# Kernel optimization log

Hardware: AMD Instinct MI355X
Metric: run time of the kernel (lower is better)

## Reference

```python
import math
import jax, jax.numpy as jnp
import numpy as np

B, L, HID = 2, 2048, 2048
H = 16
D = HID // H  # 128
EPS = 1e-6
ROPE_BASE = 10000.0
BETA_MIN, BETA_MAX = 0.8, 0.9995


def _rope_cache(seq_len, dim):
    half = dim // 2
    inv_freq = 1.0 / (ROPE_BASE ** (jnp.arange(half, dtype=jnp.float32) / float(half)))
    t = jnp.arange(seq_len, dtype=jnp.float32)
    freqs = t[:, None] * inv_freq[None, :]  # [L, half]
    return jnp.cos(freqs), jnp.sin(freqs)


def _apply_rope(x, cos, sin):
    # x: [B, H, L, D]; cos/sin: [L, D//2]
    half = x.shape[-1] // 2
    xe, xo = x[..., :half], x[..., half:]
    c = cos[None, None]
    s = sin[None, None]
    return jnp.concatenate([xe * c - xo * s, xe * s + xo * c], axis=-1)


def setup_inputs() -> dict:
    key = jax.random.key(0)
    ks = jax.random.split(key, 6)
    sc = 1.0 / math.sqrt(HID)  # ~ xavier scale
    return {
        "x": jax.random.normal(ks[0], (B, L, HID), jnp.float32),
        "Wq": jax.random.normal(ks[1], (HID, HID), jnp.float32) * sc,
        "Wk": jax.random.normal(ks[2], (HID, HID), jnp.float32) * sc,
        "Wv": jax.random.normal(ks[3], (HID, HID), jnp.float32) * sc,
        "Wg": jax.random.normal(ks[4], (HID, H), jnp.float32) * sc,
        "bg": jnp.full((H,), math.log(0.98 / (1.0 - 0.98)), jnp.float32),
        "Wo": jax.random.normal(ks[5], (HID, HID), jnp.float32) * sc,
        "bo": jnp.zeros((HID,), jnp.float32),
    }


def _deltanet(x, Wq, Wk, Wv, Wg, bg, Wo, bo):
    Bb, Ll, _ = x.shape
    split = lambda t: t.reshape(Bb, Ll, H, D).transpose(0, 2, 1, 3)  # [B,H,L,D]
    q = split(x @ Wq)
    k = split(x @ Wk)
    v = split(x @ Wv)

    cos, sin = _rope_cache(Ll, D)
    q = _apply_rope(q, cos, sin)
    k = _apply_rope(k, cos, sin)

    beta = jax.nn.sigmoid(x @ Wg + bg)                # [B,L,H]
    beta = jnp.clip(beta, BETA_MIN, BETA_MAX).transpose(0, 2, 1)  # [B,H,L]

    phi_q = jax.nn.elu(q) + 1.0
    phi_k = jax.nn.elu(k) + 1.0

    # time-major for scan
    pq = phi_q.transpose(2, 0, 1, 3)  # [L,B,H,D]
    pk = phi_k.transpose(2, 0, 1, 3)
    vt = v.transpose(2, 0, 1, 3)
    bt = beta.transpose(2, 0, 1)      # [L,B,H]

    S0 = jnp.zeros((Bb, H, D, D), jnp.float32)
    z0 = jnp.zeros((Bb, H, D), jnp.float32)

    def step(carry, inp):
        S, z = carry
        pq_t, pk_t, v_t, b_t = inp
        S = S * b_t[..., None, None] + pk_t[..., :, None] * v_t[..., None, :]
        z = z * b_t[..., None] + pk_t
        numer = jnp.einsum('bhd,bhde->bhe', pq_t, S)
        denom = jnp.sum(pq_t * z, axis=-1, keepdims=True) + EPS
        return (S, z), numer / denom

    (_, _), y = jax.lax.scan(step, (S0, z0), (pq, pk, vt, bt))  # y: [L,B,H,D]
    y = y.transpose(1, 0, 2, 3).reshape(Bb, Ll, HID)  # [B,L,H*D]
    return y @ Wo + bo


def reference(x, Wq, Wk, Wv, Wg, bg, Wo, bo):
    return _deltanet(x, Wq, Wk, Wv, Wg, bg, Wo, bo)
```

## Files before the change

### kernel.cpp

```cpp
#include <hip/hip_runtime.h>


typedef __attribute__((ext_vector_type(8))) short short8;
typedef __attribute__((ext_vector_type(4))) float f32x4;

__device__ __forceinline__ unsigned short f2bf(float f) {
  unsigned u = __float_as_uint(f);
  u += 0x7fffu + ((u >> 16) & 1u);
  return (unsigned short)(u >> 16);
}
__device__ __forceinline__ float bf2f(unsigned short s) {
  return __uint_as_float(((unsigned)s) << 16);
}
__device__ __forceinline__ float phi_elu1(float x) {
  return x > 0.f ? x + 1.f : expf(x);
}
__device__ __forceinline__ void gl_lds16(const void* g, void* l) {
  __builtin_amdgcn_global_load_lds(
      (const __attribute__((address_space(1))) void*)g,
      (__attribute__((address_space(3))) void*)l, 16, 0, 0);
}
__device__ __forceinline__ void bar_raw() {
  asm volatile("" ::: "memory");
  __builtin_amdgcn_s_barrier();
  asm volatile("" ::: "memory");
}

__global__ __launch_bounds__(256)
void k_cast(const float* __restrict__ x, unsigned short* __restrict__ xb) {
  int i = (blockIdx.x * 256 + threadIdx.x) * 4;
  float4 f = *(const float4*)(x + i);
  uint2 p;
  p.x = (unsigned)f2bf(f.x) | ((unsigned)f2bf(f.y) << 16);
  p.y = (unsigned)f2bf(f.z) | ((unsigned)f2bf(f.w) << 16);
  *(uint2*)(xb + i) = p;
}

__global__ __launch_bounds__(256)
void k_transw(const float* __restrict__ Wq, const float* __restrict__ Wk,
              const float* __restrict__ Wv, const float* __restrict__ Wo,
              const float* __restrict__ Wg,
              unsigned short* __restrict__ Wt, unsigned short* __restrict__ Wot,
              unsigned short* __restrict__ Wgt16) {
  const int z = blockIdx.z;
  if (z == 4) {
    if (blockIdx.y != 0) return;
    int idx = blockIdx.x * 256 + threadIdx.x;
    int h = idx >> 9, k4 = (idx & 511) * 4;
    uint2 p;
    p.x = (unsigned)f2bf(Wg[(k4 + 0) * 16 + h]) | ((unsigned)f2bf(Wg[(k4 + 1) * 16 + h]) << 16);
    p.y = (unsigned)f2bf(Wg[(k4 + 2) * 16 + h]) | ((unsigned)f2bf(Wg[(k4 + 3) * 16 + h]) << 16);
    *(uint2*)(Wgt16 + (size_t)h * 2048 + k4) = p;
    return;
  }
  const float* W = (z == 0) ? Wq : (z == 1) ? Wk : (z == 2) ? Wv : Wo;
  unsigned short* out = (z < 3) ? (Wt + (size_t)z * 2048 * 2048) : Wot;
  __shared__ float tile[64][65];
  const int n0 = blockIdx.x * 64;
  const int k0 = blockIdx.y * 64;
  const int tx = threadIdx.x & 63;
  const int ty = threadIdx.x >> 6;
#pragma unroll
  for (int rl = 0; rl < 16; ++rl) {
    int kk = rl * 4 + ty;
    tile[kk][tx] = W[(size_t)(k0 + kk) * 2048 + n0 + tx];
  }
  __syncthreads();
#pragma unroll
  for (int rl = 0; rl < 16; ++rl) {
    int nn = rl * 4 + ty;
    out[(size_t)(n0 + nn) * 2048 + k0 + tx] = f2bf(tile[tx][nn]);
  }
}

__global__ __launch_bounds__(256)
void k_betaW(const unsigned short* __restrict__ xb, const unsigned short* __restrict__ Wgt16,
             const float* __restrict__ bg, float* __restrict__ beta) {
  const int w = threadIdx.x >> 6;
  const int lane = threadIdx.x & 63;
  const int m = blockIdx.x * 4 + w;
  const int h = lane & 15, kq = lane >> 4;
  const unsigned short* xr = xb + (size_t)m * 2048 + kq * 512;
  const unsigned short* wr = Wgt16 + (size_t)h * 2048 + kq * 512;
  float acc = 0.f;
#pragma unroll 8
  for (int i = 0; i < 64; ++i) {
    short8 xv = *(const short8*)(xr + i * 8);
    short8 wv = *(const short8*)(wr + i * 8);
#pragma unroll
    for (int j = 0; j < 8; ++j)
      acc = fmaf(bf2f((unsigned short)xv[j]), bf2f((unsigned short)wv[j]), acc);
  }
  acc += __shfl_xor(acc, 16, 64);
  acc += __shfl_xor(acc, 32, 64);
  if (lane < 16) {
    float v = acc + bg[h];
    float bv = 1.f / (1.f + expf(-v));
    beta[(size_t)m * 16 + h] = fminf(fmaxf(bv, 0.8f), 0.9995f);
  }
}

template <bool OUT_BF16, bool ADD_BIAS>
__global__ __launch_bounds__(512, 2)
void k_gemm2(const unsigned short* __restrict__ A, const unsigned short* __restrict__ Bt,
             void* __restrict__ Cptr, const float* __restrict__ bias,
             int M, int N, int K, int ldA, int ldC) {
  __shared__ __align__(16) unsigned short Ls[3][3][128][64];
  const int tid = threadIdx.x;
  const int lane = tid & 63;
  const int w = tid >> 6;
  const int wm = w >> 1;
  const int wn = w & 1;
  const int ql = lane >> 4;
  const int r = lane & 15;

  const int nwg = gridDim.x * gridDim.y;
  const int orig = blockIdx.y * gridDim.x + blockIdx.x;
  const int li = (orig & 7) * (nwg >> 3) + (orig >> 3);
  const int m0 = (li & 15) * 256;
  const int n0 = (li >> 4) * 128;

  const int srow = tid >> 3;
  const int sphys = tid & 7;
  const int slog = sphys ^ (srow & 7);
  const unsigned short* Ab = A + (size_t)(m0 + srow) * ldA + slog * 8;
  const unsigned short* Bb = Bt + (size_t)(n0 + srow) * K + slog * 8;

#define STG(st, h, tt)                                                        \
  do {                                                                        \
    const size_t ldx = ((h) == 2) ? (size_t)K : (size_t)ldA;                  \
    const unsigned short* gs =                                                \
        (((h) == 2) ? Bb : (Ab + (size_t)((h) * 128) * ldA)) +                \
        (size_t)(tt) * 64;                                                    \
    unsigned short* ld = &Ls[(st)][(h)][srow][sphys * 8];                     \
    gl_lds16(gs, ld);                                                         \
    gl_lds16(gs + 64 * ldx, ld + 64 * 64);                                    \
  } while (0)

  f32x4 acc[4][4];
#pragma unroll
  for (int i = 0; i < 4; ++i)
#pragma unroll
    for (int j = 0; j < 4; ++j) acc[i][j] = (f32x4){0.f, 0.f, 0.f, 0.f};

  const int NT = K >> 6;

#pragma unroll
  for (int h = 0; h < 3; ++h) STG(0, h, 0);
#pragma unroll
  for (int h = 0; h < 3; ++h) STG(1, h, 1);
  asm volatile("s_waitcnt vmcnt(6)" ::: "memory");
  bar_raw();

  short8 bfr[4][2];

  for (int t = 0; t < NT; ++t) {
    const int st = t % 3;
    const unsigned short (*LA)[64] = Ls[st][wm >> 1];
    const unsigned short (*LB)[64] = Ls[st][2];
    const int arow0 = (wm & 1) * 64;
    const int brow0 = wn * 64;
    const bool pf = (t + 2 < NT);
    const int s2 = (t + 2) % 3;
#pragma unroll
    for (int p = 0; p < 2; ++p) {
      if (p == 0) {
#pragma unroll
        for (int nj = 0; nj < 4; ++nj)
#pragma unroll
          for (int kk = 0; kk < 2; ++kk)
            bfr[nj][kk] = *(const short8*)
                &LB[brow0 + nj * 16 + r][((kk * 4 + ql) ^ (r & 7)) * 8];
      }
      short8 af[2][2];
#pragma unroll
      for (int im = 0; im < 2; ++im)
#pragma unroll
        for (int kk = 0; kk < 2; ++kk)
          af[im][kk] = *(const short8*)
              &LA[arow0 + (p * 2 + im) * 16 + r][((kk * 4 + ql) ^ (r & 7)) * 8];
      if (pf) {
        if (p == 0) {
          STG(s2, 0, t + 2);
          STG(s2, 1, t + 2);
        } else {
          STG(s2, 2, t + 2);
        }
      }
      bar_raw();
      asm volatile("s_waitcnt lgkmcnt(0)" ::: "memory");
      __builtin_amdgcn_sched_barrier(0);
      __builtin_amdgcn_s_setprio(1);
#pragma unroll
      for (int kk = 0; kk < 2; ++kk)
#pragma unroll
        for (int im = 0; im < 2; ++im)
#pragma unroll
          for (int nj = 0; nj < 4; ++nj)
            acc[p * 2 + im][nj] = __builtin_amdgcn_mfma_f32_16x16x32_bf16(
                af[im][kk], bfr[nj][kk], acc[p * 2 + im][nj], 0, 0, 0);
      __builtin_amdgcn_s_setprio(0);
      if (p == 1) {
        if (pf)
          asm volatile("s_waitcnt vmcnt(6)" ::: "memory");
        else if (t + 1 < NT)
          asm volatile("s_waitcnt vmcnt(0)" ::: "memory");
      }
      bar_raw();
    }
  }
#undef STG

#pragma unroll
  for (int mi = 0; mi < 4; ++mi) {
#pragma unroll
    for (int nj = 0; nj < 4; ++nj) {
#pragma unroll
      for (int rr = 0; rr < 4; ++rr) {
        int mrow = m0 + wm * 64 + mi * 16 + ql * 4 + rr;
        int ncol = n0 + wn * 64 + nj * 16 + r;
        float val = acc[mi][nj][rr];
        if (ADD_BIAS) val += bias[ncol];
        if (OUT_BF16)
          ((unsigned short*)Cptr)[(size_t)mrow * ldC + ncol] = f2bf(val);
        else
          ((float*)Cptr)[(size_t)mrow * ldC + ncol] = val;
      }
    }
  }
}

__global__ __launch_bounds__(256)
void k_prep(const unsigned short* __restrict__ qkv, const float* __restrict__ beta,
            unsigned short* __restrict__ Qt, unsigned short* __restrict__ Ktg,
            unsigned short* __restrict__ Ag, float* __restrict__ gch) {
  const int ch = blockIdx.x;
  const int bh = blockIdx.y;
  const int b = bh >> 4, h = bh & 15;
  const int tid = threadIdx.x;
  const int t0 = ch * 64;

  __shared__ float Gs[64];
  __shared__ unsigned short Qs[64][136];
  __shared__ unsigned short Ks[64][136];

  if (tid < 64) {
    float bb = beta[((size_t)(b * 2048 + t0 + tid)) * 16 + h];
#pragma unroll
    for (int off = 1; off < 64; off <<= 1) {
      float o = __shfl_up(bb, off, 64);
      if (tid >= off) bb *= o;
    }
    Gs[tid] = bb;
    if (tid == 63) gch[bh * 32 + ch] = bb;
  }
  __syncthreads();

  const int dgl = tid & 7;
  float invf[8];
#pragma unroll
  for (int j = 0; j < 8; ++j)
    invf[j] = expf((float)(dgl * 8 + j) * -0.14391156831212787f);

  int s = tid >> 3;
#pragma unroll
  for (int rep = 0; rep < 2; ++rep, s += 32) {
    size_t row = ((size_t)(b * 2048 + t0 + s)) * 6144 + (size_t)h * 128;
    short8 qlo = *(const short8*)(qkv + row + dgl * 8);
    short8 qhi = *(const short8*)(qkv + row + 64 + dgl * 8);
    short8 klo = *(const short8*)(qkv + row + 2048 + dgl * 8);
    short8 khi = *(const short8*)(qkv + row + 2048 + 64 + dgl * 8);
    float g = Gs[s];
    float ig = 1.f / g;
    float tg = (float)(t0 + s);
    short8 oql, oqh, okl, okh;
#pragma unroll
    for (int j = 0; j < 8; ++j) {
      float sn, cs;
      __sincosf(tg * invf[j], &sn, &cs);
      float qe = bf2f((unsigned short)qlo[j]), qo = bf2f((unsigned short)qhi[j]);
      float a0 = qe * cs - qo * sn, a1 = qe * sn + qo * cs;
      oql[j] = (short)f2bf(phi_elu1(a0) * g);
      oqh[j] = (short)f2bf(phi_elu1(a1) * g);
      float ke = bf2f((unsigned short)klo[j]), ko = bf2f((unsigned short)khi[j]);
      a0 = ke * cs - ko * sn;
      a1 = ke * sn + ko * cs;
      okl[j] = (short)f2bf(phi_elu1(a0) * ig);
      okh[j] = (short)f2bf(phi_elu1(a1) * ig);
    }
    size_t qbase = (((size_t)bh * 32 + ch) * 64 + s) * 128;
    *(short8*)(Qt + qbase + dgl * 8) = oql;
    *(short8*)(Qt + qbase + 64 + dgl * 8) = oqh;
    *(short8*)&Qs[s][dgl * 8] = oql;
    *(short8*)&Qs[s][64 + dgl * 8] = oqh;
    *(short8*)&Ks[s][dgl * 8] = okl;
    *(short8*)&Ks[s][64 + dgl * 8] = okh;
  }
  __syncthreads();

  {
    const int d = tid >> 1, sh = tid & 1;
    unsigned pk[16];
#pragma unroll
    for (int i = 0; i < 16; ++i)
      pk[i] = (unsigned)Ks[sh * 32 + 2 * i][d] | ((unsigned)Ks[sh * 32 + 2 * i + 1][d] << 16);
    unsigned short* kr = Ktg + ((size_t)bh * 32 + ch) * 8192 + (size_t)d * 64 + sh * 32;
#pragma unroll
    for (int i = 0; i < 4; ++i)
      *(uint4*)(kr + i * 8) = *(uint4*)&pk[i * 4];
  }

  {
    const int lane = tid & 63;
    const int w = tid >> 6;
    const int q = lane >> 4, r = lane & 15;
    f32x4 acc[4];
#pragma unroll
    for (int nt = 0; nt < 4; ++nt) acc[nt] = (f32x4){0.f, 0.f, 0.f, 0.f};
#pragma unroll
    for (int kk = 0; kk < 4; ++kk) {
      short8 af = *(const short8*)&Qs[w * 16 + r][kk * 32 + q * 8];
#pragma unroll
      for (int nt = 0; nt < 4; ++nt) {
        short8 bf = *(const short8*)&Ks[nt * 16 + r][kk * 32 + q * 8];
        acc[nt] = __builtin_amdgcn_mfma_f32_16x16x32_bf16(af, bf, acc[nt], 0, 0, 0);
      }
    }
    unsigned short* Agp = Ag + ((size_t)bh * 32 + ch) * 4096;
#pragma unroll
    for (int nt = 0; nt < 4; ++nt) {
#pragma unroll
      for (int rr = 0; rr < 4; ++rr) {
        int t_l = w * 16 + q * 4 + rr;
        int s_l = nt * 16 + r;
        float val = (s_l <= t_l) ? acc[nt][rr] : 0.f;
        Agp[t_l * 64 + s_l] = f2bf(val);
      }
    }
  }
}

__global__ __launch_bounds__(256)
void k_scan(const unsigned short* __restrict__ Qt, const unsigned short* __restrict__ Ktg,
            const unsigned short* __restrict__ Ag, const unsigned short* __restrict__ qkv,
            const float* __restrict__ gch, unsigned short* __restrict__ numerb) {
  const int eb = blockIdx.x;
  const int bh = blockIdx.y;
  const int b = bh >> 4, h = bh & 15;
  const int tid = threadIdx.x;
  const int lane = tid & 63;
  const int w = tid >> 6;
  const int q = lane >> 4, r = lane & 15;
  const int e0 = eb * 16;

  __shared__ unsigned short Qs[64][136];
  __shared__ unsigned short Kts[128][72];
  __shared__ unsigned short As[64][72];
  __shared__ unsigned short Vt[16][72];
  __shared__ unsigned short SbT[16][136];
  __shared__ __align__(16) float zbuf[2][128];

  f32x4 S_acc[2];
  S_acc[0] = (f32x4){0.f, 0.f, 0.f, 0.f};
  S_acc[1] = (f32x4){0.f, 0.f, 0.f, 0.f};
  if (tid < 128) zbuf[0][tid] = 0.f;

  for (int ch = 0; ch < 32; ++ch) {
    const int cur = ch & 1, nxt = cur ^ 1;
    __syncthreads();
    {
      const unsigned short* Qg = Qt + ((size_t)bh * 32 + ch) * 8192;
#pragma unroll
      for (int i = 0; i < 4; ++i) {
        int c = tid + i * 256;
        int ss = c >> 4, dg = c & 15;
        *(int4*)&Qs[ss][dg * 8] = *(const int4*)(Qg + ss * 128 + dg * 8);
      }
      const unsigned short* Kg = Ktg + ((size_t)bh * 32 + ch) * 8192;
#pragma unroll
      for (int i = 0; i < 4; ++i) {
        int c = tid + i * 256;
        int d = c >> 3, sg = c & 7;
        *(int4*)&Kts[d][sg * 8] = *(const int4*)(Kg + d * 64 + sg * 8);
      }
      const unsigned short* Agp = Ag + ((size_t)bh * 32 + ch) * 4096;
#pragma unroll
      for (int i = 0; i < 2; ++i) {
        int c = tid + i * 256;
        int t_l = c >> 3, sg = c & 7;
        *(int4*)&As[t_l][sg * 8] = *(const int4*)(Agp + t_l * 64 + sg * 8);
      }
      {
        int ss = tid >> 2, e4 = tid & 3;
        const unsigned short* vp =
            qkv + ((size_t)(b * 2048 + ch * 64 + ss)) * 6144 + 4096 + h * 128 + e0 + e4 * 4;
        uint2 vv = *(const uint2*)vp;
        const unsigned short* pv = (const unsigned short*)&vv;
#pragma unroll
        for (int j = 0; j < 4; ++j) Vt[e4 * 4 + j][ss] = pv[j];
      }
#pragma unroll
      for (int i = 0; i < 2; ++i)
#pragma unroll
        for (int rr = 0; rr < 4; ++rr)
          SbT[r][(2 * w + i) * 16 + q * 4 + rr] = f2bf(S_acc[i][rr]);
    }
    __syncthreads();

    const float gc = gch[bh * 32 + ch];

    f32x4 nacc = (f32x4){0.f, 0.f, 0.f, 0.f};
    float dsum = 0.f;
#pragma unroll
    for (int kk = 0; kk < 4; ++kk) {
      short8 af = *(const short8*)&Qs[w * 16 + r][kk * 32 + q * 8];
      short8 bf = *(const short8*)&SbT[r][kk * 32 + q * 8];
      nacc = __builtin_amdgcn_mfma_f32_16x16x32_bf16(af, bf, nacc, 0, 0, 0);
      const float* zp = &zbuf[cur][kk * 32 + q * 8];
      float4 z0a = *(const float4*)zp;
      float4 z0b = *(const float4*)(zp + 4);
      dsum = fmaf(bf2f((unsigned short)af[0]), z0a.x, dsum);
      dsum = fmaf(bf2f((unsigned short)af[1]), z0a.y, dsum);
      dsum = fmaf(bf2f((unsigned short)af[2]), z0a.z, dsum);
      dsum = fmaf(bf2f((unsigned short)af[3]), z0a.w, dsum);
      dsum = fmaf(bf2f((unsigned short)af[4]), z0b.x, dsum);
      dsum = fmaf(bf2f((unsigned short)af[5]), z0b.y, dsum);
      dsum = fmaf(bf2f((unsigned short)af[6]), z0b.z, dsum);
      dsum = fmaf(bf2f((unsigned short)af[7]), z0b.w, dsum);
    }
    short8 vf[2];
#pragma unroll
    for (int kk = 0; kk < 2; ++kk) {
      vf[kk] = *(const short8*)&Vt[r][kk * 32 + q * 8];
      short8 af = *(const short8*)&As[w * 16 + r][kk * 32 + q * 8];
      nacc = __builtin_amdgcn_mfma_f32_16x16x32_bf16(af, vf[kk], nacc, 0, 0, 0);
#pragma unroll
      for (int j = 0; j < 8; ++j) dsum += bf2f((unsigned short)af[j]);
    }
    dsum += __shfl_xor(dsum, 16, 64);
    dsum += __shfl_xor(dsum, 32, 64);
    float inv = 1.f / (dsum + 1e-6f);
#pragma unroll
    for (int rr = 0; rr < 4; ++rr) {
      float inv_r = __shfl(inv, q * 4 + rr, 64);
      int t_l = w * 16 + q * 4 + rr;
      size_t m = (size_t)b * 2048 + ch * 64 + t_l;
      numerb[m * 2048 + h * 128 + e0 + r] = f2bf(nacc[rr] * inv_r);
    }

    {
      int d = tid >> 1, half = tid & 1;
      const unsigned short* kp = &Kts[d][half * 32];
      float zs = 0.f;
#pragma unroll
      for (int i = 0; i < 4; ++i) {
        short8 kv = *(const short8*)(kp + i * 8);
#pragma unroll
        for (int j = 0; j < 8; ++j) zs += bf2f((unsigned short)kv[j]);
      }
      zs += __shfl_xor(zs, 1, 64);
      if (half == 0) zbuf[nxt][d] = gc * (zbuf[cur][d] + zs);
    }

#pragma unroll
    for (int i = 0; i < 2; ++i) {
#pragma unroll
      for (int kk = 0; kk < 2; ++kk) {
        short8 af = *(const short8*)&Kts[(2 * w + i) * 16 + r][kk * 32 + q * 8];
        S_acc[i] = __builtin_amdgcn_mfma_f32_16x16x32_bf16(af, vf[kk], S_acc[i], 0, 0, 0);
      }
#pragma unroll
      for (int rr = 0; rr < 4; ++rr) S_acc[i][rr] *= gc;
    }
  }
}

extern "C" void kernel_launch(void* const* d_in, const int* in_sizes, int n_in,
                              void* d_out, int out_size, void* d_ws, size_t ws_size,
                              hipStream_t stream) {
  const float* x  = (const float*)d_in[0];
  const float* Wq = (const float*)d_in[1];
  const float* Wk = (const float*)d_in[2];
  const float* Wv = (const float*)d_in[3];
  const float* Wg = (const float*)d_in[4];
  const float* bg = (const float*)d_in[5];
  const float* Wo = (const float*)d_in[6];
  const float* bo = (const float*)d_in[7];

  char* ws = (char*)d_ws;
  unsigned short* xb    = (unsigned short*)(ws);
  unsigned short* Qt    = (unsigned short*)(ws);
  unsigned short* Wt    = (unsigned short*)(ws + 16777216);
  unsigned short* Ktg   = (unsigned short*)(ws + 16777216);
  unsigned short* Ag    = (unsigned short*)(ws + 33554432);
  unsigned short* Wot   = (unsigned short*)(ws + 41943040);
  unsigned short* qkvb  = (unsigned short*)(ws + 50331648);
  float*          beta  = (float*)(ws + 100663296);
  unsigned short* Wgt16 = (unsigned short*)(ws + 101187584);
  unsigned short* numerb= (unsigned short*)(ws + 101187584);
  float*          gch   = (float*)d_out;

  k_cast<<<8192, 256, 0, stream>>>(x, xb);
  k_transw<<<dim3(32, 32, 5), 256, 0, stream>>>(Wq, Wk, Wv, Wo, Wg, Wt, Wot, Wgt16);
  k_gemm2<true, false><<<dim3(16, 48), 512, 0, stream>>>(
      xb, Wt, qkvb, nullptr, 4096, 6144, 2048, 2048, 6144);
  k_betaW<<<1024, 256, 0, stream>>>(xb, Wgt16, bg, beta);
  k_prep<<<dim3(32, 32), 256, 0, stream>>>(qkvb, beta, Qt, Ktg, Ag, gch);
  k_scan<<<dim3(8, 32), 256, 0, stream>>>(Qt, Ktg, Ag, qkvb, gch, numerb);
  k_gemm2<false, true><<<dim3(16, 16), 512, 0, stream>>>(
      numerb, Wot, d_out, bo, 4096, 2048, 2048, 2048, 2048);
}
```

Baseline: 426.6 us.

## Add 256x256-tile double-buffered GEMM for the QKV projection

Adds a new bf16 MFMA GEMM kernel with 256x256 output tiles (8 waves in a 2x4 layout, each computing 128x64) and a two-stage LDS buffer. It replaces the 256x128 triple-buffered kernel for the QKV projection, aiming for more data reuse per loaded tile and fewer global loads. It also moves the wait/sched_barrier placement in the existing GEMM so the explicit lgkmcnt wait before the MFMAs is gone. The larger tile raises register pressure (acc 8x4) and cuts the grid to 384 blocks, which may hurt occupancy and load balance.

```diff
diff --git a/kernel.cpp b/kernel.cpp
--- a/kernel.cpp
+++ b/kernel.cpp
@@ -102,6 +102,127 @@
 
 template <bool OUT_BF16, bool ADD_BIAS>
 __global__ __launch_bounds__(512, 2)
+void k_gemm256(const unsigned short* __restrict__ A, const unsigned short* __restrict__ Bt,
+               void* __restrict__ Cptr, const float* __restrict__ bias,
+               int M, int N, int K, int ldA, int ldC) {
+  __shared__ __align__(16) unsigned short Ls[2][4][128][64];
+  const int tid = threadIdx.x;
+  const int lane = tid & 63;
+  const int w = tid >> 6;
+  const int wm = w >> 2;
+  const int wn = w & 3;
+  const int ql = lane >> 4;
+  const int r = lane & 15;
+
+  const int nwg = gridDim.x * gridDim.y;
+  const int orig = blockIdx.y * gridDim.x + blockIdx.x;
+  const int li = (orig & 7) * (nwg >> 3) + (orig >> 3);
+  const int m0 = (li & 15) * 256;
+  const int n0 = (li >> 4) * 256;
+
+  const int srow = tid >> 3;
+  const int sphys = tid & 7;
+  const int slog = sphys ^ (srow & 7);
+  const unsigned short* Abase = A + (size_t)(m0 + srow) * ldA + slog * 8;
+  const unsigned short* Bbase = Bt + (size_t)(n0 + srow) * K + slog * 8;
+
+#define STAGE256(Xv)                                                          \
+  do {                                                                        \
+    const int Xh = (Xv);                                                      \
+    const int tx = Xh >> 2, jx = Xh & 3;                                      \
+    const size_t ldx = (jx < 2) ? (size_t)K : (size_t)ldA;                    \
+    const unsigned short* gsrc =                                              \
+        ((jx < 2) ? Bbase : Abase) + (size_t)((jx & 1) * 128) * ldx +         \
+        (size_t)tx * 64;                                                      \
+    unsigned short* ldst = &Ls[tx & 1][jx ^ 2][srow][sphys * 8];              \
+    gl_lds16(gsrc, ldst);                                                     \
+    gl_lds16(gsrc + 64 * ldx, ldst + 64 * 64);                                \
+  } while (0)
+
+  f32x4 acc[8][4];
+#pragma unroll
+  for (int i = 0; i < 8; ++i)
+#pragma unroll
+    for (int j = 0; j < 4; ++j) acc[i][j] = (f32x4){0.f, 0.f, 0.f, 0.f};
+
+  const int NT = K >> 6;
+
+  for (int X = 0; X < 6; ++X) STAGE256(X);
+  asm volatile("s_waitcnt vmcnt(4)" ::: "memory");
+  bar_raw();
+
+  short8 bfr[4][2];
+
+  for (int t = 0; t < NT; ++t) {
+    const int slt = t & 1;
+    const unsigned short (*LA)[64] = Ls[slt][wm];
+    const unsigned short (*LB)[64] = Ls[slt][2 + (wn >> 1)];
+    const int brow0 = (wn & 1) * 64;
+#pragma unroll
+    for (int p = 0; p < 4; ++p) {
+      if (p == 0) {
+#pragma unroll
+        for (int nj = 0; nj < 4; ++nj)
+#pragma unroll
+          for (int kk = 0; kk < 2; ++kk)
+            bfr[nj][kk] = *(const short8*)
+                &LB[brow0 + nj * 16 + r][((kk * 4 + ql) ^ (r & 7)) * 8];
+      }
+      short8 af[2][2];
+#pragma unroll
+      for (int im = 0; im < 2; ++im)
+#pragma unroll
+        for (int kk = 0; kk < 2; ++kk)
+          af[im][kk] = *(const short8*)
+              &LA[(2 * p + im) * 16 + r][((kk * 4 + ql) ^ (r & 7)) * 8];
+      {
+        const int X = 4 * t + p + 6;
+        if (X < 4 * NT) STAGE256(X);
+      }
+      bar_raw();
+      __builtin_amdgcn_s_setprio(1);
+#pragma unroll
+      for (int kk = 0; kk < 2; ++kk)
+#pragma unroll
+        for (int im = 0; im < 2; ++im)
+#pragma unroll
+          for (int nj = 0; nj < 4; ++nj)
+            acc[2 * p + im][nj] = __builtin_amdgcn_mfma_f32_16x16x32_bf16(
+                af[im][kk], bfr[nj][kk], acc[2 * p + im][nj], 0, 0, 0);
+      __builtin_amdgcn_s_setprio(0);
+      if (p == 3) {
+        if (t + 2 < NT)
+          asm volatile("s_waitcnt vmcnt(4)" ::: "memory");
+        else if (t + 1 < NT)
+          asm volatile("s_waitcnt vmcnt(0)" ::: "memory");
+      }
+      __builtin_amdgcn_sched_barrier(0);
+      bar_raw();
+    }
+  }
+#undef STAGE256
+
+#pragma unroll
+  for (int mi = 0; mi < 8; ++mi) {
+#pragma unroll
+    for (int nj = 0; nj < 4; ++nj) {
+#pragma unroll
+      for (int rr = 0; rr < 4; ++rr) {
+        int mrow = m0 + wm * 128 + mi * 16 + ql * 4 + rr;
+        int ncol = n0 + wn * 64 + nj * 16 + r;
+        float val = acc[mi][nj][rr];
+        if (ADD_BIAS) val += bias[ncol];
+        if (OUT_BF16)
+          ((unsigned short*)Cptr)[(size_t)mrow * ldC + ncol] = f2bf(val);
+        else
+          ((float*)Cptr)[(size_t)mrow * ldC + ncol] = val;
+      }
+    }
+  }
+}
+
+template <bool OUT_BF16, bool ADD_BIAS>
+__global__ __launch_bounds__(512, 2)
 void k_gemm2(const unsigned short* __restrict__ A, const unsigned short* __restrict__ Bt,
              void* __restrict__ Cptr, const float* __restrict__ bias,
              int M, int N, int K, int ldA, int ldC) {
@@ -188,8 +309,6 @@
         }
       }
       bar_raw();
-      asm volatile("s_waitcnt lgkmcnt(0)" ::: "memory");
-      __builtin_amdgcn_sched_barrier(0);
       __builtin_amdgcn_s_setprio(1);
 #pragma unroll
       for (int kk = 0; kk < 2; ++kk)
@@ -206,6 +325,7 @@
         else if (t + 1 < NT)
           asm volatile("s_waitcnt vmcnt(0)" ::: "memory");
       }
+      __builtin_amdgcn_sched_barrier(0);
       bar_raw();
     }
   }
@@ -502,7 +622,7 @@
 
   k_cast<<<8192, 256, 0, stream>>>(x, xb);
   k_transw<<<dim3(32, 32, 5), 256, 0, stream>>>(Wq, Wk, Wv, Wo, Wg, Wt, Wot, Wgt16);
-  k_gemm2<true, false><<<dim3(16, 48), 512, 0, stream>>>(
+  k_gemm256<true, false><<<dim3(24, 16), 512, 0, stream>>>(
       xb, Wt, qkvb, nullptr, 4096, 6144, 2048, 2048, 6144);
   k_betaW<<<1024, 256, 0, stream>>>(xb, Wgt16, bg, beta);
   k_prep<<<dim3(32, 32), 256, 0, stream>>>(qkvb, beta, Qt, Ktg, Ag, gch);
```

Result: no change. 428.4 us (+0.4%).
